# Kernel tuning notes

Measured on AMD Instinct MI355X. Metric: run time of the kernel, lower is better.

Reference implementation:

```python
import jax, jax.numpy as jnp
import numpy as np

D = 1024
H = 16
HD = D // H  # 64
FF = 4 * D
EPS = 1e-5


def _xavier(key, shape):
    fan_in, fan_out = shape[1], shape[0]
    limit = float(np.sqrt(6.0 / (fan_in + fan_out)))
    return jax.random.uniform(key, shape, jnp.float32, -limit, limit)


def setup_inputs() -> dict:
    key = jax.random.key(0)
    ks = jax.random.split(key, 8)
    x = jax.random.normal(ks[0], (2, 2048, D), jnp.float32)
    return {
        "x": x,
        "w_qkv": _xavier(ks[1], (3 * D, D)),
        "b_qkv": jnp.zeros((3 * D,), jnp.float32),
        "w_out": _xavier(ks[2], (D, D)),
        "b_out": jnp.zeros((D,), jnp.float32),
        "w1": _xavier(ks[3], (FF, D)),
        "b1": jnp.zeros((FF,), jnp.float32),
        "w2": _xavier(ks[4], (D, FF)),
        "b2": jnp.zeros((D,), jnp.float32),
        "ln1_g": jnp.ones((D,), jnp.float32),
        "ln1_b": jnp.zeros((D,), jnp.float32),
        "ln2_g": jnp.ones((D,), jnp.float32),
        "ln2_b": jnp.zeros((D,), jnp.float32),
    }


def _layernorm(x, g, b):
    mu = jnp.mean(x, -1, keepdims=True)
    var = jnp.mean(jnp.square(x - mu), -1, keepdims=True)
    return (x - mu) * jax.lax.rsqrt(var + EPS) * g + b


def reference(x, w_qkv, b_qkv, w_out, b_out, w1, b1, w2, b2,
              ln1_g, ln1_b, ln2_g, ln2_b):
    B, S, _ = x.shape
    # pre-LN attention branch
    h = _layernorm(x, ln1_g, ln1_b)
    qkv = h @ w_qkv.T + b_qkv                      # [B,S,3D]
    qkv = qkv.reshape(B, S, H, 3 * HD).transpose(0, 2, 1, 3)  # [B,H,S,3hd]
    q, k, v = jnp.split(qkv, 3, axis=-1)
    scores = jnp.einsum('bhqd,bhkd->bhqk', q, k) / np.sqrt(HD)
    attn = jax.nn.softmax(scores, axis=-1)
    ctx = jnp.einsum('bhqk,bhkd->bhqd', attn, v)   # [B,H,S,hd]
    ctx = ctx.transpose(0, 2, 1, 3).reshape(B, S, D)
    x = x + (ctx @ w_out.T + b_out)
    # pre-LN MLP branch
    h = _layernorm(x, ln2_g, ln2_b)
    h = jax.nn.relu(h @ w1.T + b1)
    x = x + (h @ w2.T + b2)
    return x
```

## Files before the change

### kernel.cpp

```cpp
#include <hip/hip_runtime.h>
#include <hip/hip_bf16.h>

typedef __attribute__((ext_vector_type(8))) short bf16x8;
typedef __attribute__((ext_vector_type(4))) float f32x4;
typedef __attribute__((ext_vector_type(16))) float f32x16;
typedef __attribute__((ext_vector_type(4))) unsigned short u16x4;
typedef __attribute__((ext_vector_type(4))) unsigned int u32x4;
typedef unsigned short u16;

__device__ __forceinline__ u16 f2bf(float f) {
  unsigned u = __builtin_bit_cast(unsigned, f);
  u += 0x7fffu + ((u >> 16) & 1u);
  return (u16)(u >> 16);
}
__device__ __forceinline__ float bf2f(u16 u) {
  unsigned v = ((unsigned)u) << 16;
  return __builtin_bit_cast(float, v);
}
__device__ __forceinline__ unsigned cvt_pk_bf16(float lo, float hi) {
  unsigned r;
  asm("v_cvt_pk_bf16_f32 %0, %1, %2" : "=v"(r) : "v"(lo), "v"(hi));
  return r;
}
__device__ __forceinline__ float exp2_fast(float x) {
  float r;
  asm("v_exp_f32 %0, %1" : "=v"(r) : "v"(x));
  return r;
}

__device__ __forceinline__ void gl_lds16(const void* g, void* l) {
  __builtin_amdgcn_global_load_lds((const __attribute__((address_space(1))) void*)g,
                                   (__attribute__((address_space(3))) void*)l,
                                   16, 0, 0);
}

__device__ __forceinline__ void bar() {
  asm volatile("" ::: "memory");
  __builtin_amdgcn_s_barrier();
  asm volatile("" ::: "memory");
}

__global__ __launch_bounds__(256) void ln_cvt(const float* __restrict__ x,
                                              const float* __restrict__ g,
                                              const float* __restrict__ b,
                                              u16* __restrict__ out,
                                              const float* __restrict__ wa,
                                              const float* __restrict__ wb,
                                              const float* __restrict__ wc,
                                              const float* __restrict__ wd,
                                              u16* __restrict__ oa,
                                              u16* __restrict__ ob,
                                              u16* __restrict__ oc,
                                              u16* __restrict__ od) {
  __shared__ float red[8];
  const int t = threadIdx.x;
  if (blockIdx.x < 4096) {
    const int row = blockIdx.x;
    const int lane = t & 63, w = t >> 6;
    const float4 v = ((const float4*)(x + (size_t)row * 1024))[t];
    float s = v.x + v.y + v.z + v.w;
    float q = v.x * v.x + v.y * v.y + v.z * v.z + v.w * v.w;
#pragma unroll
    for (int off = 32; off; off >>= 1) {
      s += __shfl_down(s, off);
      q += __shfl_down(q, off);
    }
    if (lane == 0) { red[w] = s; red[4 + w] = q; }
    __syncthreads();
    s = red[0] + red[1] + red[2] + red[3];
    q = red[4] + red[5] + red[6] + red[7];
    const float mu = s * (1.f / 1024.f);
    const float var = q * (1.f / 1024.f) - mu * mu;
    const float rs = rsqrtf(var + 1e-5f);
    const float4 gv = ((const float4*)g)[t];
    const float4 bv = ((const float4*)b)[t];
    u16x4 o;
    o.x = f2bf((v.x - mu) * rs * gv.x + bv.x);
    o.y = f2bf((v.y - mu) * rs * gv.y + bv.y);
    o.z = f2bf((v.z - mu) * rs * gv.z + bv.z);
    o.w = f2bf((v.w - mu) * rs * gv.w + bv.w);
    ((u16x4*)(out + (size_t)row * 1024))[t] = o;
  } else {
    int i = (blockIdx.x - 4096) * 256 + t;
    const int stride = 2048 * 256;
    for (; i < 3145728; i += stride) {
      const float* src;
      u16* dst;
      int j;
      if (i < 786432) { src = wa; dst = oa; j = i; }
      else if (i < 1048576) { src = wb; dst = ob; j = i - 786432; }
      else if (i < 2097152) { src = wc; dst = oc; j = i - 1048576; }
      else { src = wd; dst = od; j = i - 2097152; }
      float4 v = ((const float4*)src)[j];
      u16x4 o;
      o.x = f2bf(v.x); o.y = f2bf(v.y); o.z = f2bf(v.z); o.w = f2bf(v.w);
      ((u16x4*)dst)[j] = o;
    }
  }
}

__global__ __launch_bounds__(256) void ln_k(const float* __restrict__ x,
                                            const float* __restrict__ g,
                                            const float* __restrict__ b,
                                            u16* __restrict__ out) {
  const int row = blockIdx.x;
  const int t = threadIdx.x;
  const int lane = t & 63, w = t >> 6;
  const float4 v = ((const float4*)(x + (size_t)row * 1024))[t];
  float s = v.x + v.y + v.z + v.w;
  float q = v.x * v.x + v.y * v.y + v.z * v.z + v.w * v.w;
#pragma unroll
  for (int off = 32; off; off >>= 1) {
    s += __shfl_down(s, off);
    q += __shfl_down(q, off);
  }
  __shared__ float red[8];
  if (lane == 0) { red[w] = s; red[4 + w] = q; }
  __syncthreads();
  s = red[0] + red[1] + red[2] + red[3];
  q = red[4] + red[5] + red[6] + red[7];
  const float mu = s * (1.f / 1024.f);
  const float var = q * (1.f / 1024.f) - mu * mu;
  const float rs = rsqrtf(var + 1e-5f);
  const float4 gv = ((const float4*)g)[t];
  const float4 bv = ((const float4*)b)[t];
  u16x4 o;
  o.x = f2bf((v.x - mu) * rs * gv.x + bv.x);
  o.y = f2bf((v.y - mu) * rs * gv.y + bv.y);
  o.z = f2bf((v.z - mu) * rs * gv.z + bv.z);
  o.w = f2bf((v.w - mu) * rs * gv.w + bv.w);
  ((u16x4*)(out + (size_t)row * 1024))[t] = o;
}

template <int BM, int BN, int BK, int TH, int WN, int MR, int NR, int EPI>
__global__ __launch_bounds__(TH, 2) void gemm_rot(const u16* __restrict__ A,
                                                  const u16* __restrict__ B,
                                                  const float* __restrict__ bias,
                                                  const float* __restrict__ res,
                                                  void* __restrict__ outp,
                                                  const int N, const int K) {
  constexpr int GPR = BK / 8;
  constexpr int KS = BK / 32;
  constexpr int AELEMS = BM * BK;
  constexpr int BELEMS = BN * BK;
  constexpr int NC = (BM + BN) * GPR / TH;
  static_assert((BM * GPR) % TH == 0 && ((BM + BN) * GPR) % TH == 0, "");
  __shared__ u16 lds[3][AELEMS + BELEMS];
  const int t = threadIdx.x;
  const int lane = t & 63, w = t >> 6;
  const int wm = w / WN, wn = w % WN;
  const int l15 = lane & 15, lhi = lane >> 4;
  const int nbx = gridDim.x;
  const int nwg = nbx * gridDim.y;
  const int orig = blockIdx.y * nbx + blockIdx.x;
  const int cpx = nwg >> 3;
  const int lid = (orig & 7) * cpx + (orig >> 3);
  const long bm = (long)(lid / nbx) * BM, bn = (long)(lid % nbx) * BN;
  const u16* Ab = A + bm * K;
  const u16* Bb = B + bn * K;
  const int nk = K / BK;

#define STAGE(kt_, bufi)                                                      \
  do {                                                                        \
    const long kk_ = (long)(kt_) * BK;                                        \
    _Pragma("unroll")                                                         \
    for (int j = 0; j < NC; ++j) {                                            \
      const int sj = j * TH + t;                                              \
      const u16* src_;                                                        \
      if ((j + 1) * TH <= BM * GPR) {                                         \
        const int row_ = sj / GPR, grp_ = sj % GPR;                           \
        const int g_ = (BK == 32) ? (grp_ ^ ((row_ >> 1) & 3))                \
                                  : (grp_ ^ (row_ & 7));                      \
        src_ = Ab + (size_t)row_ * K + kk_ + g_ * 8;                          \
      } else {                                                                \
        const int sb_ = sj - BM * GPR;                                        \
        const int row_ = sb_ / GPR, grp_ = sb_ % GPR;                         \
        const int g_ = (BK == 32) ? (grp_ ^ ((row_ >> 1) & 3))                \
                                  : (grp_ ^ (row_ & 7));                      \
        src_ = Bb + (size_t)row_ * K + kk_ + g_ * 8;                          \
      }                                                                       \
      gl_lds16(src_, &lds[bufi][(size_t)(j * TH + w * 64) * 8]);              \
    }                                                                         \
  } while (0)

  f32x4 acc[MR][NR] = {};
  STAGE(0, 0);
  STAGE(1, 1);
  for (int i = 0; i < nk; ++i) {
    if (i + 1 < nk) {
      if constexpr (NC == 3)      asm volatile("s_waitcnt vmcnt(3)" ::: "memory");
      else if constexpr (NC == 4) asm volatile("s_waitcnt vmcnt(4)" ::: "memory");
      else                        asm volatile("s_waitcnt vmcnt(6)" ::: "memory");
    } else {
      asm volatile("s_waitcnt vmcnt(0)" ::: "memory");
    }
    bar();
    if (i + 2 < nk) STAGE(i + 2, (i + 2) % 3);
    const u16* bufA = lds[i % 3];
    const u16* bufB = bufA + AELEMS;
    bf16x8 av[MR][KS], bv[NR][KS];
#pragma unroll
    for (int ii = 0; ii < MR; ++ii) {
      const int R = wm * (MR * 16) + ii * 16 + l15;
#pragma unroll
      for (int ks = 0; ks < KS; ++ks) {
        const int pos = (BK == 32) ? (lhi ^ ((R >> 1) & 3))
                                   : ((ks * 4 + lhi) ^ (R & 7));
        av[ii][ks] = *(const bf16x8*)&bufA[R * BK + (pos << 3)];
      }
    }
#pragma unroll
    for (int jj = 0; jj < NR; ++jj) {
      const int R = wn * (NR * 16) + jj * 16 + l15;
#pragma unroll
      for (int ks = 0; ks < KS; ++ks) {
        const int pos = (BK == 32) ? (lhi ^ ((R >> 1) & 3))
                                   : ((ks * 4 + lhi) ^ (R & 7));
        bv[jj][ks] = *(const bf16x8*)&bufB[R * BK + (pos << 3)];
      }
    }
    __builtin_amdgcn_s_setprio(1);
#pragma unroll
    for (int ii = 0; ii < MR; ++ii)
#pragma unroll
      for (int jj = 0; jj < NR; ++jj)
#pragma unroll
        for (int ks = 0; ks < KS; ++ks)
          acc[ii][jj] = __builtin_amdgcn_mfma_f32_16x16x32_bf16(av[ii][ks], bv[jj][ks],
                                                                acc[ii][jj], 0, 0, 0);
    __builtin_amdgcn_s_setprio(0);
  }
#undef STAGE
#pragma unroll
  for (int jj = 0; jj < NR; ++jj) {
    const long col = bn + wn * (NR * 16) + jj * 16 + l15;
    const float bj = bias[col];
#pragma unroll
    for (int ii = 0; ii < MR; ++ii) {
      const long row0 = bm + wm * (MR * 16) + ii * 16 + lhi * 4;
#pragma unroll
      for (int r = 0; r < 4; ++r) {
        const float v = acc[ii][jj][r] + bj;
        const long idx = (row0 + r) * N + col;
        if constexpr (EPI == 0) {
          ((u16*)outp)[idx] = f2bf(v);
        } else if constexpr (EPI == 1) {
          ((float*)outp)[idx] = v + res[idx];
        } else {
          ((u16*)outp)[idx] = f2bf(v > 0.f ? v : 0.f);
        }
      }
    }
  }
}

__global__ __launch_bounds__(256) void vtrans(const u16* __restrict__ qkv,
                                              u16* __restrict__ vt) {
  const int t = threadIdx.x;
  const int bh = blockIdx.y, b = bh >> 4, h = bh & 15;
  const int kvb = blockIdx.x * 64;
  __shared__ u16 tile[64][72];
  const u16* src = qkv + ((size_t)(b * 2048 + kvb)) * 3072 + h * 192 + 128;
#pragma unroll
  for (int rr = 0; rr < 2; ++rr) {
    const int e = rr * 2048 + t * 8;
    const int kv = e >> 6, d = e & 63;
    *(bf16x8*)&tile[kv][d] = *(const bf16x8*)(src + (size_t)kv * 3072 + d);
  }
  __syncthreads();
#pragma unroll
  for (int rr = 0; rr < 2; ++rr) {
    const int e = rr * 2048 + t * 8;
    const int d = e >> 6, kv = e & 63;
    bf16x8 o;
#pragma unroll
    for (int j = 0; j < 8; ++j) o[j] = (short)tile[kv + j][d];
    *(bf16x8*)(vt + ((size_t)bh * 64 + d) * 2048 + kvb + kv) = o;
  }
}

__global__ __launch_bounds__(256, 4) void attn_k(const u16* __restrict__ qkv,
                                                 const u16* __restrict__ vt,
                                                 u16* __restrict__ part0,
                                                 u16* __restrict__ part1,
                                                 float* __restrict__ lbuf) {
  __shared__ u16 kt[2][4096];
  __shared__ u16 vtl[2][4096];
  const int t = threadIdx.x;
  const int lane = t & 63, w = t >> 6;
  const int l31 = lane & 31, hl = lane >> 5;
  const int l7 = l31 & 7;
  const int bh = blockIdx.y, b = bh >> 4, h = bh & 15;
  const int qb = blockIdx.x * 128 + w * 32;
  const int sidx = blockIdx.z;
  const int kvbeg = sidx * 1024, kvend = kvbeg + 1024;

  const float qscale = 0.125f * 1.44269504f;
  const u16* qp = qkv + ((size_t)(b * 2048 + qb + l31)) * 3072 + h * 192;
  bf16x8 qf[4];
#pragma unroll
  for (int ds = 0; ds < 4; ++ds) {
    bf16x8 v = *(const bf16x8*)(qp + 16 * ds + 8 * hl);
#pragma unroll
    for (int j = 0; j < 8; ++j) v[j] = (short)f2bf(bf2f((u16)v[j]) * qscale);
    qf[ds] = v;
  }
  bf16x8 ones;
#pragma unroll
  for (int j = 0; j < 8; ++j) ones[j] = (short)0x3F80;

  const int srow = t >> 3, sgc = t & 7;
  const int sswz = (sgc ^ (srow & 7)) * 8;
  const u16* kg0 = qkv + ((size_t)(b * 2048 + srow)) * 3072 + h * 192 + 64 + sswz;
  const u16* vg0 = vt + (size_t)bh * 64 * 2048 + (size_t)srow * 2048 + sswz;

  f32x16 o0 = {}, o1 = {}, ol = {};

#define STAGE(bufi, kv0i)                                              \
  do {                                                                 \
    const u16* ks_ = kg0 + (size_t)(kv0i) * 3072;                      \
    const u16* vs_ = vg0 + (kv0i);                                     \
    gl_lds16(ks_, &kt[bufi][w * 512]);                                 \
    gl_lds16(ks_ + (size_t)32 * 3072, &kt[bufi][2048 + w * 512]);      \
    gl_lds16(vs_, &vtl[bufi][w * 512]);                                \
    gl_lds16(vs_ + (size_t)32 * 2048, &vtl[bufi][2048 + w * 512]);     \
  } while (0)

#define PACK(dst, SA, tl)                                                 \
  do {                                                                    \
    unsigned A0 = cvt_pk_bf16(SA[8 * tl + 0], SA[8 * tl + 1]);            \
    unsigned A1 = cvt_pk_bf16(SA[8 * tl + 2], SA[8 * tl + 3]);            \
    unsigned B0 = cvt_pk_bf16(SA[8 * tl + 4], SA[8 * tl + 5]);            \
    unsigned B1 = cvt_pk_bf16(SA[8 * tl + 6], SA[8 * tl + 7]);            \
    asm volatile("v_permlane32_swap_b32 %0, %1" : "+v"(A0), "+v"(B0));    \
    asm volatile("v_permlane32_swap_b32 %0, %1" : "+v"(A1), "+v"(B1));    \
    u32x4 pv_ = {A0, A1, B0, B1};                                         \
    dst = __builtin_bit_cast(bf16x8, pv_);                                \
  } while (0)

  int buf = 0;
  STAGE(0, kvbeg);
  for (int kv0 = kvbeg; kv0 < kvend; kv0 += 64) {
    asm volatile("s_waitcnt vmcnt(0)" ::: "memory");
    bar();
    if (kv0 + 64 < kvend) STAGE(buf ^ 1, kv0 + 64);
    f32x16 sa0 = {}, sa1 = {};
    __builtin_amdgcn_s_setprio(1);
#pragma unroll
    for (int ds = 0; ds < 4; ++ds) {
      const bf16x8 kf0 = *(const bf16x8*)&kt[buf][l31 * 64 + (((2 * ds + hl) ^ l7) << 3)];
      const bf16x8 kf1 = *(const bf16x8*)&kt[buf][(32 + l31) * 64 + (((2 * ds + hl) ^ l7) << 3)];
      sa0 = __builtin_amdgcn_mfma_f32_32x32x16_bf16(kf0, qf[ds], sa0, 0, 0, 0);
      sa1 = __builtin_amdgcn_mfma_f32_32x32x16_bf16(kf1, qf[ds], sa1, 0, 0, 0);
    }
    __builtin_amdgcn_s_setprio(0);
#pragma unroll
    for (int i = 0; i < 16; ++i) sa0[i] = exp2_fast(sa0[i]);
#pragma unroll
    for (int i = 0; i < 16; ++i) sa1[i] = exp2_fast(sa1[i]);
    bf16x8 pf0, pf1, pf2, pf3;
    PACK(pf0, sa0, 0);
    PACK(pf1, sa0, 1);
    PACK(pf2, sa1, 0);
    PACK(pf3, sa1, 1);
    __builtin_amdgcn_s_setprio(1);
#pragma unroll
    for (int t4i = 0; t4i < 4; ++t4i) {
      const bf16x8 vf0 = *(const bf16x8*)&vtl[buf][l31 * 64 + (((2 * t4i + hl) ^ l7) << 3)];
      const bf16x8 vf1 = *(const bf16x8*)&vtl[buf][(32 + l31) * 64 + (((2 * t4i + hl) ^ l7) << 3)];
      const bf16x8 pf = (t4i == 0) ? pf0 : (t4i == 1) ? pf1 : (t4i == 2) ? pf2 : pf3;
      o0 = __builtin_amdgcn_mfma_f32_32x32x16_bf16(vf0, pf, o0, 0, 0, 0);
      o1 = __builtin_amdgcn_mfma_f32_32x32x16_bf16(vf1, pf, o1, 0, 0, 0);
      ol = __builtin_amdgcn_mfma_f32_32x32x16_bf16(ones, pf, ol, 0, 0, 0);
    }
    __builtin_amdgcn_s_setprio(0);
    buf ^= 1;
  }
#undef STAGE
#undef PACK
  bar();
  if (lane < 32) {
    lbuf[(size_t)(sidx * 32 + bh) * 2048 + qb + l31] = ol[0];
  }
  u16* obase = (sidx == 0) ? part0 : part1;
  u16* ow = ((u16*)kt) + w * 2048;
#pragma unroll
  for (int g2 = 0; g2 < 4; ++g2) {
    uint2 v0, v1;
    v0.x = cvt_pk_bf16(o0[4 * g2 + 0], o0[4 * g2 + 1]);
    v0.y = cvt_pk_bf16(o0[4 * g2 + 2], o0[4 * g2 + 3]);
    v1.x = cvt_pk_bf16(o1[4 * g2 + 0], o1[4 * g2 + 1]);
    v1.y = cvt_pk_bf16(o1[4 * g2 + 2], o1[4 * g2 + 3]);
    *(uint2*)&ow[l31 * 64 + ((g2 ^ l7) << 3) + hl * 4] = v0;
    *(uint2*)&ow[l31 * 64 + (((4 + g2) ^ l7) << 3) + hl * 4] = v1;
  }
#pragma unroll
  for (int p = 0; p < 4; ++p) {
    const int q = 8 * p + (lane >> 3);
    const int gpos = lane & 7;
    const bf16x8 val = *(const bf16x8*)&ow[q * 64 + (gpos << 3)];
    const int gd = gpos ^ (q & 7);
    *(bf16x8*)(obase + ((size_t)(b * 2048 + qb + q)) * 1024 + h * 64 + gd * 8) = val;
  }
}

__global__ __launch_bounds__(256) void attn_merge(const u16* __restrict__ p1,
                                                  const float* __restrict__ lbuf,
                                                  u16* __restrict__ ctx) {
  const int c = blockIdx.x * 256 + threadIdx.x;
  const int row = c >> 7;
  const int b = row >> 11, q = row & 2047;
  const int h = (c >> 3) & 15;
  const int bh = b * 16 + h;
  const float l1 = lbuf[(size_t)bh * 2048 + q];
  const float l2 = lbuf[(size_t)(32 + bh) * 2048 + q];
  const float inv = 1.f / (l1 + l2);
  const bf16x8 v0 = ((const bf16x8*)ctx)[c];
  const bf16x8 v1 = ((const bf16x8*)p1)[c];
  float r[8];
#pragma unroll
  for (int j = 0; j < 8; ++j)
    r[j] = (bf2f((u16)v0[j]) + bf2f((u16)v1[j])) * inv;
  u32x4 ov = {cvt_pk_bf16(r[0], r[1]), cvt_pk_bf16(r[2], r[3]),
              cvt_pk_bf16(r[4], r[5]), cvt_pk_bf16(r[6], r[7])};
  ((u32x4*)ctx)[c] = ov;
}

extern "C" void kernel_launch(void* const* d_in, const int* in_sizes, int n_in,
                              void* d_out, int out_size, void* d_ws, size_t ws_size,
                              hipStream_t stream) {
  const float* x     = (const float*)d_in[0];
  const float* w_qkv = (const float*)d_in[1];
  const float* b_qkv = (const float*)d_in[2];
  const float* w_out = (const float*)d_in[3];
  const float* b_out = (const float*)d_in[4];
  const float* w1    = (const float*)d_in[5];
  const float* b1    = (const float*)d_in[6];
  const float* w2    = (const float*)d_in[7];
  const float* b2    = (const float*)d_in[8];
  const float* ln1g  = (const float*)d_in[9];
  const float* ln1b  = (const float*)d_in[10];
  const float* ln2g  = (const float*)d_in[11];
  const float* ln2b  = (const float*)d_in[12];
  float* out = (float*)d_out;

  u16* wqkv_b = (u16*)d_ws;
  u16* wout_b = wqkv_b + (size_t)3072 * 1024;
  u16* w1_b   = wout_b + (size_t)1024 * 1024;
  u16* w2_b   = w1_b + (size_t)4096 * 1024;
  u16* r1     = w2_b + (size_t)1024 * 4096;
  u16* r2     = r1 + (size_t)4096 * 1024;
  u16* qkvb   = r2;
  u16* vtb    = r2 + (size_t)4096 * 3072;
  float* x2   = (float*)(r2 + (size_t)4096 * 4096);
  u16* part1  = (u16*)x2;
  float* lbuf = (float*)(part1 + (size_t)4096 * 1024);

  ln_cvt<<<6144, 256, 0, stream>>>(x, ln1g, ln1b, r1,
                                   w_qkv, w_out, w1, w2,
                                   wqkv_b, wout_b, w1_b, w2_b);

  gemm_rot<128, 256, 32, 512, 4, 4, 4, 0><<<dim3(12, 32), 512, 0, stream>>>(
      r1, wqkv_b, b_qkv, nullptr, qkvb, 3072, 1024);
  vtrans<<<dim3(32, 32), 256, 0, stream>>>(qkvb, vtb);
  attn_k<<<dim3(16, 32, 2), 256, 0, stream>>>(qkvb, vtb, r1, part1, lbuf);
  attn_merge<<<2048, 256, 0, stream>>>(part1, lbuf, r1);
  gemm_rot<64, 128, 64, 256, 2, 2, 4, 1><<<dim3(8, 64), 256, 0, stream>>>(
      r1, wout_b, b_out, x, x2, 1024, 1024);
  ln_k<<<4096, 256, 0, stream>>>(x2, ln2g, ln2b, r1);
  gemm_rot<128, 256, 32, 512, 4, 4, 4, 2><<<dim3(16, 32), 512, 0, stream>>>(
      r1, w1_b, b1, nullptr, r2, 4096, 1024);
  gemm_rot<64, 128, 64, 256, 2, 2, 4, 1><<<dim3(8, 64), 256, 0, stream>>>(
      r2, w2_b, b2, x2, out, 1024, 4096);
}
```

Baseline: 213.3 us.

## Retile GEMMs, double-buffer LDS, stage bf16 epilogue via LDS, enlarge attention blocks

The GEMM kernel drops from triple to double LDS buffering with a full vmcnt(0) wait each iteration and raises the occupancy hint to 3 blocks. Its bf16 epilogue now stages the tile through swizzled LDS and writes 16-byte vectors instead of scattered 2-byte stores. The QKV and FFN1 GEMMs move to 128x128x64 tiles with 256 threads. The attention kernel uses 512-thread blocks covering 256 queries with a remapped block index, and computes the softmax denominator by summing in registers plus a shuffle instead of an extra MFMA against a ones vector. Shallower prefetch may expose more memory latency in exchange for lower LDS use and higher occupancy.

```diff
diff --git a/kernel.cpp b/kernel.cpp
--- a/kernel.cpp
+++ b/kernel.cpp
@@ -133,7 +133,7 @@
 }
 
 template <int BM, int BN, int BK, int TH, int WN, int MR, int NR, int EPI>
-__global__ __launch_bounds__(TH, 2) void gemm_rot(const u16* __restrict__ A,
+__global__ __launch_bounds__(TH, 3) void gemm_rot(const u16* __restrict__ A,
                                                   const u16* __restrict__ B,
                                                   const float* __restrict__ bias,
                                                   const float* __restrict__ res,
@@ -145,7 +145,7 @@
   constexpr int BELEMS = BN * BK;
   constexpr int NC = (BM + BN) * GPR / TH;
   static_assert((BM * GPR) % TH == 0 && ((BM + BN) * GPR) % TH == 0, "");
-  __shared__ u16 lds[3][AELEMS + BELEMS];
+  __shared__ u16 lds[2][AELEMS + BELEMS];
   const int t = threadIdx.x;
   const int lane = t & 63, w = t >> 6;
   const int wm = w / WN, wn = w % WN;
@@ -185,18 +185,11 @@
 
   f32x4 acc[MR][NR] = {};
   STAGE(0, 0);
-  STAGE(1, 1);
   for (int i = 0; i < nk; ++i) {
-    if (i + 1 < nk) {
-      if constexpr (NC == 3)      asm volatile("s_waitcnt vmcnt(3)" ::: "memory");
-      else if constexpr (NC == 4) asm volatile("s_waitcnt vmcnt(4)" ::: "memory");
-      else                        asm volatile("s_waitcnt vmcnt(6)" ::: "memory");
-    } else {
-      asm volatile("s_waitcnt vmcnt(0)" ::: "memory");
-    }
+    asm volatile("s_waitcnt vmcnt(0)" ::: "memory");
     bar();
-    if (i + 2 < nk) STAGE(i + 2, (i + 2) % 3);
-    const u16* bufA = lds[i % 3];
+    if (i + 1 < nk) STAGE(i + 1, (i + 1) & 1);
+    const u16* bufA = lds[i & 1];
     const u16* bufB = bufA + AELEMS;
     bf16x8 av[MR][KS], bv[NR][KS];
 #pragma unroll
@@ -231,25 +224,53 @@
     __builtin_amdgcn_s_setprio(0);
   }
 #undef STAGE
-#pragma unroll
-  for (int jj = 0; jj < NR; ++jj) {
-    const long col = bn + wn * (NR * 16) + jj * 16 + l15;
-    const float bj = bias[col];
-#pragma unroll
-    for (int ii = 0; ii < MR; ++ii) {
-      const long row0 = bm + wm * (MR * 16) + ii * 16 + lhi * 4;
-#pragma unroll
-      for (int r = 0; r < 4; ++r) {
-        const float v = acc[ii][jj][r] + bj;
-        const long idx = (row0 + r) * N + col;
-        if constexpr (EPI == 0) {
-          ((u16*)outp)[idx] = f2bf(v);
-        } else if constexpr (EPI == 1) {
+  if constexpr (EPI == 1) {
+#pragma unroll
+    for (int jj = 0; jj < NR; ++jj) {
+      const long col = bn + wn * (NR * 16) + jj * 16 + l15;
+      const float bj = bias[col];
+#pragma unroll
+      for (int ii = 0; ii < MR; ++ii) {
+        const long row0 = bm + wm * (MR * 16) + ii * 16 + lhi * 4;
+#pragma unroll
+        for (int r = 0; r < 4; ++r) {
+          const float v = acc[ii][jj][r] + bj;
+          const long idx = (row0 + r) * N + col;
           ((float*)outp)[idx] = v + res[idx];
-        } else {
-          ((u16*)outp)[idx] = f2bf(v > 0.f ? v : 0.f);
         }
       }
+    }
+  } else {
+    bar();
+    constexpr int WC = NR * 16;
+    constexpr int WTOT = MR * 16 * WC;
+    u16* cw = ((u16*)lds) + w * WTOT;
+#pragma unroll
+    for (int jj = 0; jj < NR; ++jj) {
+      const long col = bn + wn * WC + jj * 16 + l15;
+      const float bj = bias[col];
+      const int cg = (jj * 16 + l15) >> 3;
+      const int co = l15 & 7;
+#pragma unroll
+      for (int ii = 0; ii < MR; ++ii) {
+#pragma unroll
+        for (int r = 0; r < 4; ++r) {
+          float v = acc[ii][jj][r] + bj;
+          if constexpr (EPI == 2) v = v > 0.f ? v : 0.f;
+          const int row = ii * 16 + lhi * 4 + r;
+          cw[row * WC + (((cg ^ (row & 7)) << 3) | co)] = f2bf(v);
+        }
+      }
+    }
+    const long rowbase = bm + wm * (MR * 16);
+    const long colbase = bn + wn * WC;
+#pragma unroll
+    for (int p = 0; p < WTOT / 512; ++p) {
+      const int idx = p * 512 + lane * 8;
+      const int row = idx / WC;
+      const int cg2 = (idx % WC) >> 3;
+      const bf16x8 val = *(const bf16x8*)&cw[row * WC + ((cg2 ^ (row & 7)) << 3)];
+      *(bf16x8*)&((u16*)outp)[(rowbase + row) * N + colbase + cg2 * 8] = val;
     }
   }
 }
@@ -279,21 +300,23 @@
   }
 }
 
-__global__ __launch_bounds__(256, 4) void attn_k(const u16* __restrict__ qkv,
+__global__ __launch_bounds__(512, 4) void attn_k(const u16* __restrict__ qkv,
                                                  const u16* __restrict__ vt,
                                                  u16* __restrict__ part0,
                                                  u16* __restrict__ part1,
                                                  float* __restrict__ lbuf) {
-  __shared__ u16 kt[2][4096];
-  __shared__ u16 vtl[2][4096];
+  __shared__ u16 smem[16384];
   const int t = threadIdx.x;
   const int lane = t & 63, w = t >> 6;
   const int l31 = lane & 31, hl = lane >> 5;
   const int l7 = l31 & 7;
-  const int bh = blockIdx.y, b = bh >> 4, h = bh & 15;
-  const int qb = blockIdx.x * 128 + w * 32;
-  const int sidx = blockIdx.z;
-  const int kvbeg = sidx * 1024, kvend = kvbeg + 1024;
+  const int lid = blockIdx.x + 8 * blockIdx.y + 256 * blockIdx.z;
+  const int bh = (lid & 7) * 4 + ((lid >> 3) & 3);
+  const int qblk = (lid >> 5) & 7;
+  const int sidx = lid >> 8;
+  const int b = bh >> 4, h = bh & 15;
+  const int qb = qblk * 256 + w * 32;
+  const int kvbeg = sidx * 1024;
 
   const float qscale = 0.125f * 1.44269504f;
   const u16* qp = qkv + ((size_t)(b * 2048 + qb + l31)) * 3072 + h * 192;
@@ -305,25 +328,19 @@
     for (int j = 0; j < 8; ++j) v[j] = (short)f2bf(bf2f((u16)v[j]) * qscale);
     qf[ds] = v;
   }
-  bf16x8 ones;
-#pragma unroll
-  for (int j = 0; j < 8; ++j) ones[j] = (short)0x3F80;
 
   const int srow = t >> 3, sgc = t & 7;
   const int sswz = (sgc ^ (srow & 7)) * 8;
   const u16* kg0 = qkv + ((size_t)(b * 2048 + srow)) * 3072 + h * 192 + 64 + sswz;
   const u16* vg0 = vt + (size_t)bh * 64 * 2048 + (size_t)srow * 2048 + sswz;
 
-  f32x16 o0 = {}, o1 = {}, ol = {};
+  f32x16 o0 = {}, o1 = {};
+  float lsum = 0.f;
 
 #define STAGE(bufi, kv0i)                                              \
   do {                                                                 \
-    const u16* ks_ = kg0 + (size_t)(kv0i) * 3072;                      \
-    const u16* vs_ = vg0 + (kv0i);                                     \
-    gl_lds16(ks_, &kt[bufi][w * 512]);                                 \
-    gl_lds16(ks_ + (size_t)32 * 3072, &kt[bufi][2048 + w * 512]);      \
-    gl_lds16(vs_, &vtl[bufi][w * 512]);                                \
-    gl_lds16(vs_ + (size_t)32 * 2048, &vtl[bufi][2048 + w * 512]);     \
+    gl_lds16(kg0 + (size_t)(kv0i) * 3072, &smem[(bufi) * 4096 + w * 512]); \
+    gl_lds16(vg0 + (kv0i), &smem[8192 + (bufi) * 4096 + w * 512]);     \
   } while (0)
 
 #define PACK(dst, SA, tl)                                                 \
@@ -340,16 +357,18 @@
 
   int buf = 0;
   STAGE(0, kvbeg);
-  for (int kv0 = kvbeg; kv0 < kvend; kv0 += 64) {
+  for (int it = 0; it < 16; ++it) {
     asm volatile("s_waitcnt vmcnt(0)" ::: "memory");
     bar();
-    if (kv0 + 64 < kvend) STAGE(buf ^ 1, kv0 + 64);
+    if (it + 1 < 16) STAGE(buf ^ 1, kvbeg + (it + 1) * 64);
+    const u16* kbuf = &smem[buf * 4096];
+    const u16* vbuf = &smem[8192 + buf * 4096];
     f32x16 sa0 = {}, sa1 = {};
     __builtin_amdgcn_s_setprio(1);
 #pragma unroll
     for (int ds = 0; ds < 4; ++ds) {
-      const bf16x8 kf0 = *(const bf16x8*)&kt[buf][l31 * 64 + (((2 * ds + hl) ^ l7) << 3)];
-      const bf16x8 kf1 = *(const bf16x8*)&kt[buf][(32 + l31) * 64 + (((2 * ds + hl) ^ l7) << 3)];
+      const bf16x8 kf0 = *(const bf16x8*)&kbuf[l31 * 64 + (((2 * ds + hl) ^ l7) << 3)];
+      const bf16x8 kf1 = *(const bf16x8*)&kbuf[(32 + l31) * 64 + (((2 * ds + hl) ^ l7) << 3)];
       sa0 = __builtin_amdgcn_mfma_f32_32x32x16_bf16(kf0, qf[ds], sa0, 0, 0, 0);
       sa1 = __builtin_amdgcn_mfma_f32_32x32x16_bf16(kf1, qf[ds], sa1, 0, 0, 0);
     }
@@ -358,6 +377,15 @@
     for (int i = 0; i < 16; ++i) sa0[i] = exp2_fast(sa0[i]);
 #pragma unroll
     for (int i = 0; i < 16; ++i) sa1[i] = exp2_fast(sa1[i]);
+    const f32x16 ps = sa0 + sa1;
+    float s8[8];
+#pragma unroll
+    for (int i = 0; i < 8; ++i) s8[i] = ps[i] + ps[i + 8];
+    const float q0s = (s8[0] + s8[1]) + (s8[2] + s8[3]);
+    const float q1s = (s8[4] + s8[5]) + (s8[6] + s8[7]);
+    float rsum = q0s + q1s;
+    rsum += __shfl_xor(rsum, 32);
+    lsum += rsum;
     bf16x8 pf0, pf1, pf2, pf3;
     PACK(pf0, sa0, 0);
     PACK(pf1, sa0, 1);
@@ -366,12 +394,11 @@
     __builtin_amdgcn_s_setprio(1);
 #pragma unroll
     for (int t4i = 0; t4i < 4; ++t4i) {
-      const bf16x8 vf0 = *(const bf16x8*)&vtl[buf][l31 * 64 + (((2 * t4i + hl) ^ l7) << 3)];
-      const bf16x8 vf1 = *(const bf16x8*)&vtl[buf][(32 + l31) * 64 + (((2 * t4i + hl) ^ l7) << 3)];
+      const bf16x8 vf0 = *(const bf16x8*)&vbuf[l31 * 64 + (((2 * t4i + hl) ^ l7) << 3)];
+      const bf16x8 vf1 = *(const bf16x8*)&vbuf[(32 + l31) * 64 + (((2 * t4i + hl) ^ l7) << 3)];
       const bf16x8 pf = (t4i == 0) ? pf0 : (t4i == 1) ? pf1 : (t4i == 2) ? pf2 : pf3;
       o0 = __builtin_amdgcn_mfma_f32_32x32x16_bf16(vf0, pf, o0, 0, 0, 0);
       o1 = __builtin_amdgcn_mfma_f32_32x32x16_bf16(vf1, pf, o1, 0, 0, 0);
-      ol = __builtin_amdgcn_mfma_f32_32x32x16_bf16(ones, pf, ol, 0, 0, 0);
     }
     __builtin_amdgcn_s_setprio(0);
     buf ^= 1;
@@ -380,10 +407,10 @@
 #undef PACK
   bar();
   if (lane < 32) {
-    lbuf[(size_t)(sidx * 32 + bh) * 2048 + qb + l31] = ol[0];
+    lbuf[(size_t)(sidx * 32 + bh) * 2048 + qb + l31] = lsum;
   }
   u16* obase = (sidx == 0) ? part0 : part1;
-  u16* ow = ((u16*)kt) + w * 2048;
+  u16* ow = &smem[w * 2048];
 #pragma unroll
   for (int g2 = 0; g2 < 4; ++g2) {
     uint2 v0, v1;
@@ -460,15 +487,15 @@
                                    w_qkv, w_out, w1, w2,
                                    wqkv_b, wout_b, w1_b, w2_b);
 
-  gemm_rot<128, 256, 32, 512, 4, 4, 4, 0><<<dim3(12, 32), 512, 0, stream>>>(
+  gemm_rot<128, 128, 64, 256, 2, 4, 4, 0><<<dim3(24, 32), 256, 0, stream>>>(
       r1, wqkv_b, b_qkv, nullptr, qkvb, 3072, 1024);
   vtrans<<<dim3(32, 32), 256, 0, stream>>>(qkvb, vtb);
-  attn_k<<<dim3(16, 32, 2), 256, 0, stream>>>(qkvb, vtb, r1, part1, lbuf);
+  attn_k<<<dim3(8, 32, 2), 512, 0, stream>>>(qkvb, vtb, r1, part1, lbuf);
   attn_merge<<<2048, 256, 0, stream>>>(part1, lbuf, r1);
   gemm_rot<64, 128, 64, 256, 2, 2, 4, 1><<<dim3(8, 64), 256, 0, stream>>>(
       r1, wout_b, b_out, x, x2, 1024, 1024);
   ln_k<<<4096, 256, 0, stream>>>(x2, ln2g, ln2b, r1);
-  gemm_rot<128, 256, 32, 512, 4, 4, 4, 2><<<dim3(16, 32), 512, 0, stream>>>(
+  gemm_rot<128, 128, 64, 256, 2, 4, 4, 2><<<dim3(32, 32), 256, 0, stream>>>(
       r1, w1_b, b1, nullptr, r2, 4096, 1024);
   gemm_rot<64, 128, 64, 256, 2, 2, 4, 1><<<dim3(8, 64), 256, 0, stream>>>(
       r2, w2_b, b2, x2, out, 1024, 4096);
```

Measured after the change: 207.7 us. -2.6%, faster.
